# Kernel optimization log

Hardware: AMD Instinct MI355X
Metric: run time of the kernel (lower is better)

The kernel has to match this reference:

```python
import jax, jax.numpy as jnp
import numpy as np

B, L, D, N = 8, 2048, 1024, 16


def setup_inputs() -> dict:
    key = jax.random.key(0)
    ks = jax.random.split(key, 7)
    x = jax.random.normal(ks[0], (B, L, D), dtype=jnp.float32)
    # A = -rand(d_model, d_state) - 0.5  -> in (-1.5, -0.5)
    A = -jax.random.uniform(ks[1], (D, N), dtype=jnp.float32) - 0.5
    # nn.Linear(d_model, d_state, bias=False): weight [N, D]
    Wb = jax.random.normal(ks[2], (N, D), dtype=jnp.float32) / np.sqrt(D)
    C = jax.random.normal(ks[3], (D, N), dtype=jnp.float32) * 0.1
    Dp = jax.random.normal(ks[4], (D,), dtype=jnp.float32) * 0.1
    # nn.Linear(d_model, d_model): weight [D, D], bias [D]
    Wd = jax.random.normal(ks[5], (D, D), dtype=jnp.float32) / np.sqrt(D)
    bd = jax.random.normal(ks[6], (D,), dtype=jnp.float32) * 0.01
    return {"x": x, "A": A, "Wb": Wb, "C": C, "Dp": Dp, "Wd": Wd, "bd": bd}


def reference(x, A, Wb, C, Dp, Wd, bd):
    # Precompute input-dependent projections for all timesteps (batched GEMMs)
    dt = jax.nn.softplus(jnp.einsum('bld,ed->ble', x, Wd) + bd)  # [B,L,D]
    Bx = jnp.einsum('bld,nd->bln', x, Wb)                        # [B,L,N]

    def step(h, inp):
        dt_t, bx_t, x_t = inp                  # [B,D], [B,N], [B,D]
        dA = dt_t[..., None] * A               # [B,D,N]
        h = jnp.exp(dA) * h + dt_t[..., None] * bx_t[:, None, :]
        y = jnp.einsum('bdn,dn->bd', h, C) + Dp * x_t
        return h, y

    h0 = jnp.zeros((x.shape[0], A.shape[0], A.shape[1]), dtype=x.dtype)
    xs = (jnp.swapaxes(dt, 0, 1), jnp.swapaxes(Bx, 0, 1), jnp.swapaxes(x, 0, 1))
    _, ys = jax.lax.scan(step, h0, xs)         # ys: [L,B,D]
    return jnp.swapaxes(ys, 0, 1)              # [B,L,D]
```

## Files before the change

### kernel.cpp

```cpp
#include <hip/hip_runtime.h>
#include <hip/hip_bf16.h>
#include <stdint.h>

#define B_ 8
#define L_ 2048
#define D_ 1024
#define N_ 16
#define M_ (B_ * L_)
#define K_ D_
#define SEG_ 64
#define SLEN_ (L_ / SEG_)
#define LOG2E 1.44269504088896341f

typedef __bf16 bf16;
typedef __bf16 bf16x8 __attribute__((ext_vector_type(8)));
typedef float f32x4 __attribute__((ext_vector_type(4)));

__global__ __launch_bounds__(256) void cvt_f32_bf16(const float* __restrict__ in,
                                                    bf16* __restrict__ out, int n4) {
  int i = blockIdx.x * 256 + threadIdx.x;
  const int stride = gridDim.x * 256;
  const float4* in4 = (const float4*)in;
  uint2* out2 = (uint2*)out;
  for (; i < n4; i += stride) {
    float4 v = in4[i];
    union { bf16 h[4]; uint2 u; } p;
    p.h[0] = (bf16)v.x; p.h[1] = (bf16)v.y; p.h[2] = (bf16)v.z; p.h[3] = (bf16)v.w;
    out2[i] = p.u;
  }
}

__device__ inline void gload_lds16(const bf16* g, bf16* l) {
  __builtin_amdgcn_global_load_lds(
      (const __attribute__((address_space(1))) void*)g,
      (__attribute__((address_space(3))) void*)l, 16, 0, 0);
}

__device__ inline float softplus_f(float z) {
  return fmaxf(z, 0.f) + __logf(1.f + __expf(-fabsf(z)));
}

__global__ __launch_bounds__(256) void gemm_dt(const bf16* __restrict__ Xb,
                                               const bf16* __restrict__ Wdb,
                                               const float* __restrict__ bd,
                                               bf16* __restrict__ dtb) {
  __shared__ bf16 As[128 * 64];
  __shared__ bf16 Bs[128 * 64];
  const int tid = threadIdx.x;
  const int lane = tid & 63;
  const int wave = tid >> 6;
  const int wr = wave >> 1, wc = wave & 1;
  const int virt = (blockIdx.x & 7) * 128 + (blockIdx.x >> 3);
  const int mt = virt >> 3, nt = virt & 7;
  const int m0 = mt * 128, n0 = nt * 128;

  const bf16* ga[4];
  const bf16* gb[4];
#pragma unroll
  for (int q = 0; q < 4; ++q) {
    const int cc = tid + 256 * q;
    const int row = cc >> 3, off = (cc & 7) * 8;
    ga[q] = Xb + (size_t)(m0 + row) * K_ + off;
    gb[q] = Wdb + (size_t)(n0 + row) * K_ + off;
  }

  f32x4 acc[4][4] = {};
  const int frow = (lane & 15);
  const int kg = (lane >> 4) * 8;

  for (int kt = 0; kt < K_; kt += 64) {
#pragma unroll
    for (int q = 0; q < 4; ++q) {
      gload_lds16(ga[q] + kt, &As[(tid + 256 * q) * 8]);
      gload_lds16(gb[q] + kt, &Bs[(tid + 256 * q) * 8]);
    }
    __syncthreads();
#pragma unroll
    for (int ks = 0; ks < 2; ++ks) {
      bf16x8 af[4], bfr[4];
#pragma unroll
      for (int i = 0; i < 4; ++i)
        af[i] = *(const bf16x8*)&As[(wr * 64 + i * 16 + frow) * 64 + ks * 32 + kg];
#pragma unroll
      for (int i = 0; i < 4; ++i)
        bfr[i] = *(const bf16x8*)&Bs[(wc * 64 + i * 16 + frow) * 64 + ks * 32 + kg];
#pragma unroll
      for (int i = 0; i < 4; ++i)
#pragma unroll
        for (int j = 0; j < 4; ++j)
          acc[i][j] = __builtin_amdgcn_mfma_f32_16x16x32_bf16(af[i], bfr[j], acc[i][j], 0, 0, 0);
    }
    __syncthreads();
  }

  const int rbase = m0 + wr * 64 + (lane >> 4) * 4;
  const int cbase = n0 + wc * 64 + (lane & 15);
#pragma unroll
  for (int j = 0; j < 4; ++j) {
    const int col = cbase + j * 16;
    const float bias = bd[col];
#pragma unroll
    for (int i = 0; i < 4; ++i) {
      const int row = rbase + i * 16;
#pragma unroll
      for (int r = 0; r < 4; ++r) {
        float z = acc[i][j][r] + bias;
        dtb[(size_t)(row + r) * D_ + col] = (bf16)softplus_f(z);
      }
    }
  }
}

__global__ __launch_bounds__(256) void bx_mfma(const bf16* __restrict__ Xb,
                                               const bf16* __restrict__ Wbb,
                                               float* __restrict__ Bx) {
  const int lane = threadIdx.x & 63;
  const int wave = threadIdx.x >> 6;
  const int row0 = blockIdx.x * 64 + wave * 16;
  const int fr = lane & 15;
  const int kg = (lane >> 4) * 8;
  const bf16* ga = Xb + (size_t)(row0 + fr) * K_ + kg;
  const bf16* gb = Wbb + (size_t)fr * K_ + kg;
  f32x4 acc = {};
#pragma unroll 8
  for (int kt = 0; kt < K_; kt += 32) {
    bf16x8 af = *(const bf16x8*)(ga + kt);
    bf16x8 bf = *(const bf16x8*)(gb + kt);
    acc = __builtin_amdgcn_mfma_f32_16x16x32_bf16(af, bf, acc, 0, 0, 0);
  }
  const int orow = row0 + (lane >> 4) * 4;
  const int ocol = lane & 15;
#pragma unroll
  for (int r = 0; r < 4; ++r)
    Bx[(size_t)(orow + r) * N_ + ocol] = acc[r];
}

__global__ __launch_bounds__(256) void scan_p1(
    const bf16* __restrict__ dtb, const float* __restrict__ Bx,
    const float* __restrict__ A, bf16* __restrict__ hseg,
    float* __restrict__ stot) {
  const int tid = threadIdx.x;
  const int bi = blockIdx.x;
  const int seg = bi & 63;
  const int dtile = (bi >> 6) & 3;
  const int b = bi >> 8;
  const int d = dtile * 256 + tid;
  const int l0 = seg * SLEN_;

  __shared__ float bxs[SLEN_][N_];
  if (tid < SLEN_ * N_ / 4)
    ((float4*)bxs)[tid] = ((const float4*)(Bx + ((size_t)b * L_ + l0) * N_))[tid];

  float A2[N_];
  {
    const float4* ap = (const float4*)(A + (size_t)d * N_);
#pragma unroll
    for (int q = 0; q < 4; ++q) {
      float4 a = ap[q];
      A2[q * 4 + 0] = a.x * LOG2E; A2[q * 4 + 1] = a.y * LOG2E;
      A2[q * 4 + 2] = a.z * LOG2E; A2[q * 4 + 3] = a.w * LOG2E;
    }
  }

  const bf16* dtp = dtb + ((size_t)b * L_ + l0) * D_ + d;
  float h[N_] = {};
  float s = 0.f;
  __syncthreads();

  float cdt = (float)dtp[0];
#pragma unroll 4
  for (int i = 0; i < SLEN_; ++i) {
    const int ip = (i + 1 < SLEN_) ? i + 1 : i;
    const float ndt = (float)dtp[(size_t)ip * D_];
    s += cdt;
#pragma unroll
    for (int q = 0; q < 4; ++q) {
      const float4 bv = ((const float4*)bxs[i])[q];
      const float bvf[4] = {bv.x, bv.y, bv.z, bv.w};
#pragma unroll
      for (int j = 0; j < 4; ++j) {
        const int n = q * 4 + j;
        const float e = __builtin_amdgcn_exp2f(cdt * A2[n]);
        h[n] = fmaf(e, h[n], cdt * bvf[j]);
      }
    }
    cdt = ndt;
  }

  bf16* hp = hseg + (((size_t)b * SEG_ + seg) * D_ + d) * N_;
  union { bf16 v[16]; uint4 u[2]; } pk;
#pragma unroll
  for (int n = 0; n < N_; ++n) pk.v[n] = (bf16)h[n];
  ((uint4*)hp)[0] = pk.u[0];
  ((uint4*)hp)[1] = pk.u[1];
  stot[((size_t)b * SEG_ + seg) * D_ + d] = s;
}

__global__ __launch_bounds__(256) void scan_combine(
    const float* __restrict__ A, bf16* __restrict__ hseg,
    const float* __restrict__ stot) {
  const int tid = threadIdx.x;
  const int bi = blockIdx.x;
  const int b = bi >> 6;
  const int d = (bi & 63) * 16 + (tid >> 4);
  const int n = tid & 15;
  const float A2 = A[(size_t)d * N_ + n] * LOG2E;

  const size_t hbase = ((size_t)b * SEG_ * D_ + d) * N_ + n;
  const size_t sbase = (size_t)b * SEG_ * D_ + d;
  float g = 0.f;
  float hs = (float)hseg[hbase];
  float st = stot[sbase];
  for (int sg = 0; sg < SEG_; ++sg) {
    const int s1 = (sg + 1 < SEG_) ? sg + 1 : sg;
    const float nhs = (float)hseg[hbase + (size_t)s1 * D_ * N_];
    const float nst = stot[sbase + (size_t)s1 * D_];
    hseg[hbase + (size_t)sg * D_ * N_] = (bf16)g;
    g = fmaf(__builtin_amdgcn_exp2f(A2 * st), g, hs);
    hs = nhs; st = nst;
  }
}

__global__ __launch_bounds__(256) void scan_p3(
    const bf16* __restrict__ dtb, const float* __restrict__ Bx,
    const bf16* __restrict__ xb, const float* __restrict__ A,
    const float* __restrict__ C, const float* __restrict__ Dp,
    const bf16* __restrict__ hseg, float* __restrict__ out) {
  const int tid = threadIdx.x;
  const int bi = blockIdx.x;
  const int seg = bi & 63;
  const int dtile = (bi >> 6) & 3;
  const int b = bi >> 8;
  const int d = dtile * 256 + tid;
  const int l0 = seg * SLEN_;

  __shared__ float bxs[SLEN_][N_];
  if (tid < SLEN_ * N_ / 4)
    ((float4*)bxs)[tid] = ((const float4*)(Bx + ((size_t)b * L_ + l0) * N_))[tid];

  float A2[N_], Cv[N_], h[N_];
  {
    const float4* ap = (const float4*)(A + (size_t)d * N_);
    const float4* cp = (const float4*)(C + (size_t)d * N_);
    const bf16* hp = hseg + (((size_t)b * SEG_ + seg) * D_ + d) * N_;
    union { uint4 u[2]; bf16 v[16]; } pk;
    pk.u[0] = ((const uint4*)hp)[0];
    pk.u[1] = ((const uint4*)hp)[1];
#pragma unroll
    for (int q = 0; q < 4; ++q) {
      float4 a = ap[q], c = cp[q];
      A2[q * 4 + 0] = a.x * LOG2E; A2[q * 4 + 1] = a.y * LOG2E;
      A2[q * 4 + 2] = a.z * LOG2E; A2[q * 4 + 3] = a.w * LOG2E;
      Cv[q * 4 + 0] = c.x; Cv[q * 4 + 1] = c.y;
      Cv[q * 4 + 2] = c.z; Cv[q * 4 + 3] = c.w;
    }
#pragma unroll
    for (int n = 0; n < N_; ++n) h[n] = (float)pk.v[n];
  }
  const float Dpv = Dp[d];

  const size_t base = ((size_t)b * L_ + l0) * D_ + d;
  const bf16* dtp = dtb + base;
  const bf16* xp = xb + base;
  float* op = out + base;
  __syncthreads();

  float cdt = (float)dtp[0];
  float cx = (float)xp[0];
#pragma unroll 4
  for (int i = 0; i < SLEN_; ++i) {
    const int ip = (i + 1 < SLEN_) ? i + 1 : i;
    const float ndt = (float)dtp[(size_t)ip * D_];
    const float nx = (float)xp[(size_t)ip * D_];
    float y = Dpv * cx;
#pragma unroll
    for (int q = 0; q < 4; ++q) {
      const float4 bv = ((const float4*)bxs[i])[q];
      const float bvf[4] = {bv.x, bv.y, bv.z, bv.w};
#pragma unroll
      for (int j = 0; j < 4; ++j) {
        const int n = q * 4 + j;
        const float e = __builtin_amdgcn_exp2f(cdt * A2[n]);
        h[n] = fmaf(e, h[n], cdt * bvf[j]);
        y = fmaf(h[n], Cv[n], y);
      }
    }
    op[(size_t)i * D_] = y;
    cdt = ndt; cx = nx;
  }
}

extern "C" void kernel_launch(void* const* d_in, const int* in_sizes, int n_in,
                              void* d_out, int out_size, void* d_ws, size_t ws_size,
                              hipStream_t stream) {
  const float* x  = (const float*)d_in[0];
  const float* A  = (const float*)d_in[1];
  const float* Wb = (const float*)d_in[2];
  const float* C  = (const float*)d_in[3];
  const float* Dp = (const float*)d_in[4];
  const float* Wd = (const float*)d_in[5];
  const float* bd = (const float*)d_in[6];
  float* out = (float*)d_out;

  char* ws = (char*)d_ws;
  bf16*  dtb  = (bf16*)ws;
  bf16*  xb   = (bf16*)(ws + (size_t)33554432);
  bf16*  wdb  = (bf16*)(ws + (size_t)67108864);
  bf16*  wbb  = (bf16*)(ws + (size_t)69206016);
  float* bx   = (float*)(ws + (size_t)69238784);
  bf16*  hseg = (bf16*)(ws + (size_t)70287360);
  float* stot = (float*)(ws + (size_t)87064576);

  cvt_f32_bf16<<<2048, 256, 0, stream>>>(x, xb, M_ * K_ / 4);
  cvt_f32_bf16<<<1024, 256, 0, stream>>>(Wd, wdb, D_ * K_ / 4);
  cvt_f32_bf16<<<16, 256, 0, stream>>>(Wb, wbb, N_ * K_ / 4);
  bx_mfma<<<dim3(M_ / 64), 256, 0, stream>>>(xb, wbb, bx);
  gemm_dt<<<dim3((M_ / 128) * (D_ / 128)), 256, 0, stream>>>(xb, wdb, bd, dtb);
  scan_p1<<<dim3(B_ * 4 * SEG_), 256, 0, stream>>>(dtb, bx, A, hseg, stot);
  scan_combine<<<dim3(B_ * (D_ / 16)), 256, 0, stream>>>(A, hseg, stot);
  scan_p3<<<dim3(B_ * 4 * SEG_), 256, 0, stream>>>(dtb, bx, xb, A, C, Dp, hseg, out);
}
```

Baseline: 185.9 us.

## Double-buffer dt GEMM LDS tiles with XOR swizzle and K=32 steps

```diff
diff --git a/kernel.cpp b/kernel.cpp
--- a/kernel.cpp
+++ b/kernel.cpp
@@ -44,8 +44,8 @@
                                                const bf16* __restrict__ Wdb,
                                                const float* __restrict__ bd,
                                                bf16* __restrict__ dtb) {
-  __shared__ bf16 As[128 * 64];
-  __shared__ bf16 Bs[128 * 64];
+  __shared__ bf16 As[2][128 * 32];
+  __shared__ bf16 Bs[2][128 * 32];
   const int tid = threadIdx.x;
   const int lane = tid & 63;
   const int wave = tid >> 6;
@@ -54,44 +54,58 @@
   const int mt = virt >> 3, nt = virt & 7;
   const int m0 = mt * 128, n0 = nt * 128;
 
-  const bf16* ga[4];
-  const bf16* gb[4];
-#pragma unroll
-  for (int q = 0; q < 4; ++q) {
-    const int cc = tid + 256 * q;
-    const int row = cc >> 3, off = (cc & 7) * 8;
-    ga[q] = Xb + (size_t)(m0 + row) * K_ + off;
-    gb[q] = Wdb + (size_t)(n0 + row) * K_ + off;
+  const bf16* ga[2];
+  const bf16* gb[2];
+#pragma unroll
+  for (int q = 0; q < 2; ++q) {
+    const int c = tid + 256 * q;
+    const int row = c >> 2;
+    const int col8 = ((c & 3) ^ (row & 3)) * 8;
+    ga[q] = Xb + (size_t)(m0 + row) * K_ + col8;
+    gb[q] = Wdb + (size_t)(n0 + row) * K_ + col8;
   }
 
   f32x4 acc[4][4] = {};
   const int frow = (lane & 15);
-  const int kg = (lane >> 4) * 8;
-
-  for (int kt = 0; kt < K_; kt += 64) {
-#pragma unroll
-    for (int q = 0; q < 4; ++q) {
-      gload_lds16(ga[q] + kt, &As[(tid + 256 * q) * 8]);
-      gload_lds16(gb[q] + kt, &Bs[(tid + 256 * q) * 8]);
-    }
+  const int khalf = (lane >> 4);
+
+  int aoff[4], boff[4];
+#pragma unroll
+  for (int i = 0; i < 4; ++i) {
+    const int Ra = wr * 64 + i * 16 + frow;
+    const int Rb = wc * 64 + i * 16 + frow;
+    aoff[i] = Ra * 32 + (khalf ^ (Ra & 3)) * 8;
+    boff[i] = Rb * 32 + (khalf ^ (Rb & 3)) * 8;
+  }
+
+#define STAGE_(buf, kt)                                         \
+  {                                                             \
+    gload_lds16(ga[0] + (kt), &As[buf][tid * 8]);               \
+    gload_lds16(ga[1] + (kt), &As[buf][(tid + 256) * 8]);       \
+    gload_lds16(gb[0] + (kt), &Bs[buf][tid * 8]);               \
+    gload_lds16(gb[1] + (kt), &Bs[buf][(tid + 256) * 8]);       \
+  }
+
+  STAGE_(0, 0);
+  __syncthreads();
+
+  int cur = 0;
+  for (int t = 0; t < K_ / 32; ++t) {
+    if (t + 1 < K_ / 32) STAGE_(cur ^ 1, (t + 1) * 32);
+    bf16x8 af[4], bfr[4];
+#pragma unroll
+    for (int i = 0; i < 4; ++i) af[i] = *(const bf16x8*)&As[cur][aoff[i]];
+#pragma unroll
+    for (int i = 0; i < 4; ++i) bfr[i] = *(const bf16x8*)&Bs[cur][boff[i]];
+#pragma unroll
+    for (int i = 0; i < 4; ++i)
+#pragma unroll
+      for (int j = 0; j < 4; ++j)
+        acc[i][j] = __builtin_amdgcn_mfma_f32_16x16x32_bf16(af[i], bfr[j], acc[i][j], 0, 0, 0);
     __syncthreads();
-#pragma unroll
-    for (int ks = 0; ks < 2; ++ks) {
-      bf16x8 af[4], bfr[4];
-#pragma unroll
-      for (int i = 0; i < 4; ++i)
-        af[i] = *(const bf16x8*)&As[(wr * 64 + i * 16 + frow) * 64 + ks * 32 + kg];
-#pragma unroll
-      for (int i = 0; i < 4; ++i)
-        bfr[i] = *(const bf16x8*)&Bs[(wc * 64 + i * 16 + frow) * 64 + ks * 32 + kg];
-#pragma unroll
-      for (int i = 0; i < 4; ++i)
-#pragma unroll
-        for (int j = 0; j < 4; ++j)
-          acc[i][j] = __builtin_amdgcn_mfma_f32_16x16x32_bf16(af[i], bfr[j], acc[i][j], 0, 0, 0);
-    }
-    __syncthreads();
-  }
+    cur ^= 1;
+  }
+#undef STAGE_
 
   const int rbase = m0 + wr * 64 + (lane >> 4) * 4;
   const int cbase = n0 + wc * 64 + (lane & 15);
```

After: 174.4 us. 6.2% less time.
